# Kernel tuning notes

Measured on AMD Instinct MI355X. Metric: run time of the kernel, lower is better.

## Reference

```python
import jax, jax.numpy as jnp
import numpy as np

B, T, D, H = 2, 2048, 1024, 16
DH = D // H


def setup_inputs() -> dict:
    key = jax.random.key(0)
    ks = jax.random.split(key, 11)
    s = 1.0 / np.sqrt(D)
    return {
        "q": jax.random.normal(ks[0], (B, T, D), jnp.float32),
        "k": jax.random.normal(ks[1], (B, T, D), jnp.float32),
        "v": jax.random.normal(ks[2], (B, T, D), jnp.float32),
        "wq_w": jax.random.normal(ks[3], (D, D), jnp.float32) * s,
        "wq_b": jnp.zeros((D,), jnp.float32),
        "wk_w": jax.random.normal(ks[4], (D, D), jnp.float32) * s,
        "wk_b": jnp.zeros((D,), jnp.float32),
        "wv_w": jax.random.normal(ks[5], (D, D), jnp.float32) * s,
        "wv_b": jnp.zeros((D,), jnp.float32),
        "wo_w": jax.random.normal(ks[6], (D, D), jnp.float32) * s,
        "wo_b": jnp.zeros((D,), jnp.float32),
    }


def reference(q, k, v, wq_w, wq_b, wk_w, wk_b, wv_w, wv_b, wo_w, wo_b):
    b, t, d = q.shape
    # Linear projections (torch Linear: x @ W^T + b)
    wq = (q @ wq_w.T + wq_b).reshape(b, t, H, DH)
    wk = (k @ wk_w.T + wk_b).reshape(b, t, H, DH)
    wv = (v @ wv_w.T + wv_b).reshape(b, t, H, DH)
    # scaled dot-product attention: [b,h,t,s]
    scores = jnp.einsum('bthd,bshd->bhts', wq, wk) / jnp.sqrt(jnp.float32(DH))
    probs = jax.nn.softmax(scores, axis=-1)
    attn = jnp.einsum('bhts,bshd->bthd', probs, wv)  # [b,t,h,dh]
    attn = attn.reshape(b, t, d)
    return attn @ wo_w.T + wo_b
```

## Files before the change

### kernel.cpp

```cpp
#include <hip/hip_runtime.h>
#include <hip/hip_bf16.h>
#include <stdint.h>

#define Bn  2
#define Tn  2048
#define Dn  1024
#define Hn  16
#define DHn 64
#define Mn  (Bn*Tn)

typedef __attribute__((ext_vector_type(8))) short short8;
typedef __attribute__((ext_vector_type(4))) short short4v;
typedef __attribute__((ext_vector_type(4))) float f32x4;

__device__ __forceinline__ f32x4 fzero4() { f32x4 z = {0.f, 0.f, 0.f, 0.f}; return z; }

#define TR16(dst, a32) asm volatile("ds_read_b64_tr_b16 %0, %1" : "=v"(dst) : "v"(a32))

__global__ void cvt4_kernel(const float* __restrict__ a0, const float* __restrict__ a1,
                            const float* __restrict__ a2, const float* __restrict__ a3,
                            __hip_bfloat16* __restrict__ o0, __hip_bfloat16* __restrict__ o1,
                            __hip_bfloat16* __restrict__ o2, __hip_bfloat16* __restrict__ o3, int n)
{
    const int i = (blockIdx.x * blockDim.x + threadIdx.x) * 8;
    if (i >= n) return;
    const float* in = blockIdx.y == 0 ? a0 : (blockIdx.y == 1 ? a1 : (blockIdx.y == 2 ? a2 : a3));
    __hip_bfloat16* out = blockIdx.y == 0 ? o0 : (blockIdx.y == 1 ? o1 : (blockIdx.y == 2 ? o2 : o3));
    float4 a = *(const float4*)(in + i);
    float4 b = *(const float4*)(in + i + 4);
    union { __hip_bfloat16 h[8]; short8 u; } tmp;
    tmp.h[0] = __float2bfloat16(a.x); tmp.h[1] = __float2bfloat16(a.y);
    tmp.h[2] = __float2bfloat16(a.z); tmp.h[3] = __float2bfloat16(a.w);
    tmp.h[4] = __float2bfloat16(b.x); tmp.h[5] = __float2bfloat16(b.y);
    tmp.h[6] = __float2bfloat16(b.z); tmp.h[7] = __float2bfloat16(b.w);
    *(short8*)(out + i) = tmp.u;
}

__global__ __launch_bounds__(256, 3)
void gemm_qkv_kernel(const float* __restrict__ qa, const float* __restrict__ ka,
                     const float* __restrict__ va,
                     const __hip_bfloat16* __restrict__ wq, const __hip_bfloat16* __restrict__ wk,
                     const __hip_bfloat16* __restrict__ wv,
                     const float* __restrict__ bq_, const float* __restrict__ bk_,
                     const float* __restrict__ bv_,
                     __hip_bfloat16* __restrict__ Qp, __hip_bfloat16* __restrict__ Kp,
                     __hip_bfloat16* __restrict__ Vp)
{
    __shared__ alignas(16) short As[2][128*32];
    __shared__ alignas(16) short Bs[2][128*32];
    const int grp = blockIdx.y >> 3;
    const float* A           = grp == 0 ? qa : (grp == 1 ? ka : va);
    const __hip_bfloat16* Bw = grp == 0 ? wq : (grp == 1 ? wk : wv);
    const float* bias        = grp == 0 ? bq_ : (grp == 1 ? bk_ : bv_);
    __hip_bfloat16* C        = grp == 0 ? Qp : (grp == 1 ? Kp : Vp);
    const float scl          = grp == 0 ? 0.18033688011112042f : 1.0f;

    const int t = threadIdx.x, lane = t & 63, wave = t >> 6;
    const int wm = wave >> 1, wn = wave & 1;
    const int row0 = blockIdx.x * 128, col0 = (blockIdx.y & 7) * 128;

    f32x4 acc[4][4];
#pragma unroll
    for (int m = 0; m < 4; ++m)
#pragma unroll
        for (int n = 0; n < 4; ++n) acc[m][n] = fzero4();

    const int srow = wave*16 + (lane >> 2);
    const int skk  = (lane & 3) * 8;
    const int ldsb = wave * 1024 + (lane & 63) * 16;

    float4 ra[2][2];
    auto LOAD_A = [&](int k0) {
#pragma unroll
        for (int i = 0; i < 2; ++i) {
            const float* ap = A + (size_t)(row0 + i*64 + srow)*Dn + k0 + skk;
            ra[i][0] = *(const float4*)ap;
            ra[i][1] = *(const float4*)(ap + 4);
        }
    };
    auto WRITE_A = [&](int buf) {
#pragma unroll
        for (int i = 0; i < 2; ++i) {
            union { __hip_bfloat16 h[8]; short8 u; } w;
            w.h[0] = __float2bfloat16(ra[i][0].x); w.h[1] = __float2bfloat16(ra[i][0].y);
            w.h[2] = __float2bfloat16(ra[i][0].z); w.h[3] = __float2bfloat16(ra[i][0].w);
            w.h[4] = __float2bfloat16(ra[i][1].x); w.h[5] = __float2bfloat16(ra[i][1].y);
            w.h[6] = __float2bfloat16(ra[i][1].z); w.h[7] = __float2bfloat16(ra[i][1].w);
            *(short8*)((char*)As[buf] + i*4096 + ldsb) = w.u;
        }
    };
    auto STAGE_B = [&](int buf, int k0) {
#pragma unroll
        for (int i = 0; i < 2; ++i)
            __builtin_amdgcn_global_load_lds(
                (const __attribute__((address_space(1))) void*)(Bw + (size_t)(col0 + i*64 + srow)*Dn + k0 + skk),
                (__attribute__((address_space(3))) void*)((char*)Bs[buf] + i*4096 + wave*1024 + (lane&63)*16), 16, 0, 0);
    };

    LOAD_A(0);
    STAGE_B(0, 0);
    WRITE_A(0);
    __syncthreads();
    int cur = 0;
    for (int k0 = 0; k0 < Dn; k0 += 32) {
        const bool more = (k0 + 32 < Dn);
        if (more) { LOAD_A(k0 + 32); STAGE_B(cur ^ 1, k0 + 32); }
        short8 af[4], bf_[4];
#pragma unroll
        for (int m = 0; m < 4; ++m)
            af[m] = *(const short8*)((char*)As[cur] + (wm*64 + m*16 + (lane & 15))*64 + (lane >> 4)*16);
#pragma unroll
        for (int n = 0; n < 4; ++n)
            bf_[n] = *(const short8*)((char*)Bs[cur] + (wn*64 + n*16 + (lane & 15))*64 + (lane >> 4)*16);
        __builtin_amdgcn_s_setprio(1);
#pragma unroll
        for (int m = 0; m < 4; ++m)
#pragma unroll
            for (int n = 0; n < 4; ++n)
                acc[m][n] = __builtin_amdgcn_mfma_f32_16x16x32_bf16(af[m], bf_[n], acc[m][n], 0, 0, 0);
        __builtin_amdgcn_s_setprio(0);
        __builtin_amdgcn_sched_barrier(0);
        if (more) WRITE_A(cur ^ 1);
        __syncthreads();
        cur ^= 1;
    }

#pragma unroll
    for (int n = 0; n < 4; ++n) {
        const int col = col0 + wn*64 + n*16 + (lane & 15);
        const float bv = bias[col];
#pragma unroll
        for (int m = 0; m < 4; ++m) {
            const int rb_ = row0 + wm*64 + m*16 + (lane>>4)*4;
#pragma unroll
            for (int i = 0; i < 4; ++i)
                C[(size_t)(rb_+i)*Dn + col] = __float2bfloat16((acc[m][n][i] + bv) * scl);
        }
    }
}

__global__ __launch_bounds__(256, 4)
void gemm_out_kernel(const __hip_bfloat16* __restrict__ A,
                     const __hip_bfloat16* __restrict__ Bw,
                     const float* __restrict__ bias,
                     float* __restrict__ C)
{
    __shared__ alignas(16) short As[2][64*32];
    __shared__ alignas(16) short Bs[2][128*32];
    const int t = threadIdx.x, lane = t & 63, wave = t >> 6;
    const int wm = wave >> 1, wn = wave & 1;
    const int row0 = blockIdx.x * 64, col0 = blockIdx.y * 128;

    f32x4 acc[2][4];
#pragma unroll
    for (int m = 0; m < 2; ++m)
#pragma unroll
        for (int n = 0; n < 4; ++n) acc[m][n] = fzero4();

    const int srow = wave*16 + (lane >> 2);
    const int skk  = (lane & 3) * 8;
    const int ldsb = wave * 1024;

    auto STAGE = [&](int buf, int k0) {
        __builtin_amdgcn_global_load_lds(
            (const __attribute__((address_space(1))) void*)(A + (size_t)(row0 + srow)*Dn + k0 + skk),
            (__attribute__((address_space(3))) void*)((char*)As[buf] + ldsb), 16, 0, 0);
#pragma unroll
        for (int i = 0; i < 2; ++i)
            __builtin_amdgcn_global_load_lds(
                (const __attribute__((address_space(1))) void*)(Bw + (size_t)(col0 + i*64 + srow)*Dn + k0 + skk),
                (__attribute__((address_space(3))) void*)((char*)Bs[buf] + i*4096 + ldsb), 16, 0, 0);
    };

    STAGE(0, 0);
    __syncthreads();
    int cur = 0;
    for (int k0 = 0; k0 < Dn; k0 += 32) {
        if (k0 + 32 < Dn) STAGE(cur ^ 1, k0 + 32);
        short8 af[2], bf_[4];
#pragma unroll
        for (int m = 0; m < 2; ++m)
            af[m] = *(const short8*)((char*)As[cur] + (wm*32 + m*16 + (lane & 15))*64 + (lane >> 4)*16);
#pragma unroll
        for (int n = 0; n < 4; ++n)
            bf_[n] = *(const short8*)((char*)Bs[cur] + (wn*64 + n*16 + (lane & 15))*64 + (lane >> 4)*16);
        __builtin_amdgcn_s_setprio(1);
#pragma unroll
        for (int m = 0; m < 2; ++m)
#pragma unroll
            for (int n = 0; n < 4; ++n)
                acc[m][n] = __builtin_amdgcn_mfma_f32_16x16x32_bf16(af[m], bf_[n], acc[m][n], 0, 0, 0);
        __builtin_amdgcn_s_setprio(0);
        __syncthreads();
        cur ^= 1;
    }

#pragma unroll
    for (int n = 0; n < 4; ++n) {
        const int col = col0 + wn*64 + n*16 + (lane & 15);
        const float bv = bias[col];
#pragma unroll
        for (int m = 0; m < 2; ++m) {
            const int rb_ = row0 + wm*32 + m*16 + (lane>>4)*4;
#pragma unroll
            for (int i = 0; i < 4; ++i)
                C[(size_t)(rb_+i)*Dn + col] = acc[m][n][i] + bv;
        }
    }
}

#define VPL 1288

__global__ __launch_bounds__(256, 2)
void attn_kernel(const __hip_bfloat16* __restrict__ Q,
                 const __hip_bfloat16* __restrict__ K,
                 const __hip_bfloat16* __restrict__ V,
                 __hip_bfloat16* __restrict__ O)
{
    __shared__ alignas(16) short Vlds[2*2*4*VPL];
    const int t = threadIdx.x, lane = t & 63, wave = t >> 6;
    const int g = lane >> 4, c = lane & 15;
    const int pk = wave & 1, qh = wave >> 1;
    const int blk = (blockIdx.x & 7) * 64 + (blockIdx.x >> 3);
    const int qb = blk & 15;
    const int h  = (blk >> 4) & (Hn - 1);
    const int b  = blk >> 8;
    const size_t base = (size_t)b * Tn * Dn + (size_t)h * DHn;
    const int q0 = qb * 128 + qh * 64;

    short8 bq[4][2];
#pragma unroll
    for (int qs = 0; qs < 4; ++qs) {
        const __hip_bfloat16* qp = Q + base + (size_t)(q0 + qs*16 + c) * Dn + g*8;
        bq[qs][0] = *(const short8*)qp;
        bq[qs][1] = *(const short8*)(qp + 32);
    }
    short8 ones;
#pragma unroll
    for (int i = 0; i < 8; ++i) ones[i] = (short)0x3F80;

    f32x4 o_[4][4];
#pragma unroll
    for (int qs = 0; qs < 4; ++qs)
#pragma unroll
        for (int d = 0; d < 4; ++d) o_[qs][d] = fzero4();
    float m_[4] = {-3e38f, -3e38f, -3e38f, -3e38f};
    f32x4 lacc[4] = {fzero4(), fzero4(), fzero4(), fzero4()};

    const int vrow = t >> 3;
    const int vd0  = ((t>>1)&3)*VPL + (vrow>>2)*80 + (vrow&3)*16 + (t&1)*8;
    const int vcol = (((t>>1)&3)*16 + (t&1)*8);
    const uint32_t vbase = (uint32_t)(uintptr_t)(void*)Vlds;
    const uint32_t atr = vbase + (uint32_t)(pk*10304 + g*160 + c*8);

    short8 akA[4][2], akB[4][2];
    {
        const __hip_bfloat16* kp = K + base + (size_t)(pk*64 + c) * Dn + g*8;
#pragma unroll
        for (int sub = 0; sub < 4; ++sub)
#pragma unroll
            for (int ks = 0; ks < 2; ++ks)
                akA[sub][ks] = *(const short8*)(kp + (size_t)sub*16*Dn + ks*32);
    }

    auto ITER = [&](const short8 (&ck)[4][2], short8 (&nk)[4][2], int it) {
        const int kv0 = it * 128;
        short8 cv[2][2];
#pragma unroll
        for (int p = 0; p < 2; ++p) {
            const __hip_bfloat16* vp = V + base + (size_t)(kv0 + p*64 + vrow) * Dn + vcol;
            cv[p][0] = *(const short8*)vp;
            cv[p][1] = *(const short8*)(vp + (size_t)32*Dn);
        }
        {
            const int kvn = (it < 15) ? kv0 + 128 + pk*64 : pk*64;
            const __hip_bfloat16* kp = K + base + (size_t)(kvn + c) * Dn + g*8;
#pragma unroll
            for (int sub = 0; sub < 4; ++sub)
#pragma unroll
                for (int ks = 0; ks < 2; ++ks)
                    nk[sub][ks] = *(const short8*)(kp + (size_t)sub*16*Dn + ks*32);
        }

        short8 pa[4][2];
#pragma unroll
        for (int qs = 0; qs < 4; ++qs) {
            f32x4 s_[4];
#pragma unroll
            for (int sub = 0; sub < 4; ++sub) s_[sub] = fzero4();
            __builtin_amdgcn_s_setprio(1);
#pragma unroll
            for (int sub = 0; sub < 4; ++sub)
#pragma unroll
                for (int ks = 0; ks < 2; ++ks)
                    s_[sub] = __builtin_amdgcn_mfma_f32_16x16x32_bf16(
                        ck[sub][ks], bq[qs][ks], s_[sub], 0, 0, 0);
            __builtin_amdgcn_s_setprio(0);

            float r0 = fmaxf(fmaxf(s_[0][0], s_[0][1]), fmaxf(s_[0][2], s_[0][3]));
            float r1 = fmaxf(fmaxf(s_[1][0], s_[1][1]), fmaxf(s_[1][2], s_[1][3]));
            float r2 = fmaxf(fmaxf(s_[2][0], s_[2][1]), fmaxf(s_[2][2], s_[2][3]));
            float r3 = fmaxf(fmaxf(s_[3][0], s_[3][1]), fmaxf(s_[3][2], s_[3][3]));
            float rm = fmaxf(fmaxf(r0, r1), fmaxf(r2, r3));
            if (!__all(rm - m_[qs] <= 8.0f)) {
                float gm = fmaxf(rm, __shfl_xor(rm, 16));
                gm = fmaxf(gm, __shfl_xor(gm, 32));
                const float mn = fmaxf(m_[qs], gm);
                const float sc = exp2f(m_[qs] - mn);
                m_[qs] = mn;
                lacc[qs][0] *= sc;
#pragma unroll
                for (int d = 0; d < 4; ++d)
#pragma unroll
                    for (int i = 0; i < 4; ++i) o_[qs][d][i] *= sc;
            }
            const float mn = m_[qs];
#pragma unroll
            for (int kc = 0; kc < 2; ++kc)
#pragma unroll
                for (int hf = 0; hf < 2; ++hf)
#pragma unroll
                    for (int i = 0; i < 4; ++i) {
                        const float p = exp2f(s_[kc*2+hf][i] - mn);
                        union { __hip_bfloat16 hb; short u; } cvp;
                        cvp.hb = __float2bfloat16(p);
                        pa[qs][kc][hf*4 + i] = cvp.u;
                    }
            lacc[qs] = __builtin_amdgcn_mfma_f32_16x16x32_bf16(ones, pa[qs][0], lacc[qs], 0, 0, 0);
            lacc[qs] = __builtin_amdgcn_mfma_f32_16x16x32_bf16(ones, pa[qs][1], lacc[qs], 0, 0, 0);
        }

        short* vb = Vlds + (it & 1) * 10304;
#pragma unroll
        for (int p = 0; p < 2; ++p) {
            *(short8*)(vb + p*5152 + vd0)       = cv[p][0];
            *(short8*)(vb + p*5152 + vd0 + 640) = cv[p][1];
        }
        asm volatile("s_waitcnt lgkmcnt(0)" ::: "memory");
        __builtin_amdgcn_s_barrier();
        __builtin_amdgcn_sched_barrier(0);

        const uint32_t atrb = atr + (uint32_t)((it & 1) * 20608u);
        short4v tv[4][2][2];
#pragma unroll
        for (int d = 0; d < 4; ++d)
#pragma unroll
            for (int kc = 0; kc < 2; ++kc) {
                const uint32_t a = atrb + (uint32_t)(d*2576 + kc*1280);
                TR16(tv[d][kc][0], a);
                TR16(tv[d][kc][1], a + 640);
            }
#pragma unroll
        for (int d = 0; d < 4; ++d) {
            if (d == 0)      asm volatile("s_waitcnt lgkmcnt(12)" ::: "memory");
            else if (d == 1) asm volatile("s_waitcnt lgkmcnt(8)" ::: "memory");
            else if (d == 2) asm volatile("s_waitcnt lgkmcnt(4)" ::: "memory");
            else             asm volatile("s_waitcnt lgkmcnt(0)" ::: "memory");
            __builtin_amdgcn_sched_barrier(0);
            const short8 av0 = __builtin_shufflevector(tv[d][0][0], tv[d][0][1], 0,1,2,3,4,5,6,7);
            const short8 av1 = __builtin_shufflevector(tv[d][1][0], tv[d][1][1], 0,1,2,3,4,5,6,7);
            __builtin_amdgcn_s_setprio(1);
#pragma unroll
            for (int qs = 0; qs < 4; ++qs) {
                o_[qs][d] = __builtin_amdgcn_mfma_f32_16x16x32_bf16(av0, pa[qs][0], o_[qs][d], 0, 0, 0);
                o_[qs][d] = __builtin_amdgcn_mfma_f32_16x16x32_bf16(av1, pa[qs][1], o_[qs][d], 0, 0, 0);
            }
            __builtin_amdgcn_s_setprio(0);
        }
    };

    for (int j = 0; j < 8; ++j) {
        ITER(akA, akB, 2*j);
        ITER(akB, akA, 2*j + 1);
    }

    __syncthreads();
    float* cbase = (float*)Vlds;
    if (pk == 1) {
        float* cb = cbase + qh * 4608;
#pragma unroll
        for (int qs = 0; qs < 4; ++qs)
#pragma unroll
            for (int d = 0; d < 4; ++d)
                *(f32x4*)(cb + ((qs*4 + d)*64 + lane)*4) = o_[qs][d];
#pragma unroll
        for (int qs = 0; qs < 4; ++qs) {
            cb[4096 + qs*64 + lane] = m_[qs];
            cb[4352 + qs*64 + lane] = lacc[qs][0];
        }
    }
    __syncthreads();
    if (pk == 0) {
        float* cb = cbase + qh * 4608;
#pragma unroll
        for (int qs = 0; qs < 4; ++qs) {
            const float m1 = cb[4096 + qs*64 + lane];
            const float l1 = cb[4352 + qs*64 + lane];
            const float mN = fmaxf(m_[qs], m1);
            const float sc0 = exp2f(m_[qs] - mN);
            const float sc1 = exp2f(m1 - mN);
            const float inv = 1.f / (lacc[qs][0]*sc0 + l1*sc1);
            __hip_bfloat16* op = O + base + (size_t)(q0 + qs*16 + c) * Dn + g*4;
#pragma unroll
            for (int d = 0; d < 4; ++d) {
                const f32x4 o1 = *(const f32x4*)(cb + ((qs*4 + d)*64 + lane)*4);
                union { __hip_bfloat16 hb[4]; ushort4 u4; } w;
#pragma unroll
                for (int i = 0; i < 4; ++i)
                    w.hb[i] = __float2bfloat16((o_[qs][d][i]*sc0 + o1[i]*sc1) * inv);
                *(ushort4*)(op + d*16) = w.u4;
            }
        }
    }
}

extern "C" void kernel_launch(void* const* d_in, const int* in_sizes, int n_in,
                              void* d_out, int out_size, void* d_ws, size_t ws_size,
                              hipStream_t stream)
{
    (void)in_sizes; (void)n_in; (void)out_size; (void)ws_size;
    const float* q    = (const float*)d_in[0];
    const float* k    = (const float*)d_in[1];
    const float* v    = (const float*)d_in[2];
    const float* wq_w = (const float*)d_in[3];
    const float* wq_b = (const float*)d_in[4];
    const float* wk_w = (const float*)d_in[5];
    const float* wk_b = (const float*)d_in[6];
    const float* wv_w = (const float*)d_in[7];
    const float* wv_b = (const float*)d_in[8];
    const float* wo_w = (const float*)d_in[9];
    const float* wo_b = (const float*)d_in[10];

    char* ws = (char*)d_ws;
    const size_t S1 = (size_t)Mn * Dn * 2;
    const size_t W  = (size_t)Dn * Dn * 2;
    __hip_bfloat16* wqb = (__hip_bfloat16*)(ws);
    __hip_bfloat16* wkb = (__hip_bfloat16*)(ws + W);
    __hip_bfloat16* wvb = (__hip_bfloat16*)(ws + 2*W);
    __hip_bfloat16* wob = (__hip_bfloat16*)(ws + 3*W);
    __hip_bfloat16* Qp  = (__hip_bfloat16*)(ws + 4*W);
    __hip_bfloat16* Kp  = (__hip_bfloat16*)(ws + 4*W + S1);
    __hip_bfloat16* Vp  = (__hip_bfloat16*)(ws + 4*W + 2*S1);
    __hip_bfloat16* Ap  = (__hip_bfloat16*)(ws + 4*W + 3*S1);

    const int nW = Dn * Dn;
    cvt4_kernel<<<dim3(nW/2048, 4), 256, 0, stream>>>(wq_w, wk_w, wv_w, wo_w,
                                                      wqb, wkb, wvb, wob, nW);

    gemm_qkv_kernel<<<dim3(Mn/128, 24), 256, 0, stream>>>(
        q, k, v, wqb, wkb, wvb, wq_b, wk_b, wv_b, Qp, Kp, Vp);

    attn_kernel<<<Bn*Hn*(Tn/128), 256, 0, stream>>>(Qp, Kp, Vp, Ap);

    gemm_out_kernel<<<dim3(Mn/64, Dn/128), 256, 0, stream>>>(Ap, wob, wo_b, (float*)d_out);
}
```

Measured before the change: 134.8 us.

## Split attention KV range across two blocks and merge with combine kernel

Splits each attention block's key/value sequence into two halves, doubling the grid from 512 to 1024 blocks to better fill the GPU's compute units. Each block writes unnormalized fp32 partial outputs plus running max and sum, and a new combine kernel merges the halves and writes bf16 attention output. This trades extra global traffic (fp32 partials, about 33MB written and read back) and an extra kernel launch for more parallelism. The workspace is rearranged so the partials overlap the weight buffers that are no longer needed, and the attention output reuses the Q buffer.

```diff
diff --git a/kernel.cpp b/kernel.cpp
--- a/kernel.cpp
+++ b/kernel.cpp
@@ -215,18 +215,21 @@
 void attn_kernel(const __hip_bfloat16* __restrict__ Q,
                  const __hip_bfloat16* __restrict__ K,
                  const __hip_bfloat16* __restrict__ V,
-                 __hip_bfloat16* __restrict__ O)
+                 float* __restrict__ PO, float* __restrict__ PM, float* __restrict__ PL)
 {
     __shared__ alignas(16) short Vlds[2*2*4*VPL];
     const int t = threadIdx.x, lane = t & 63, wave = t >> 6;
     const int g = lane >> 4, c = lane & 15;
     const int pk = wave & 1, qh = wave >> 1;
-    const int blk = (blockIdx.x & 7) * 64 + (blockIdx.x >> 3);
-    const int qb = blk & 15;
-    const int h  = (blk >> 4) & (Hn - 1);
-    const int b  = blk >> 8;
+    const int blk = (blockIdx.x & 7) * 128 + (blockIdx.x >> 3);
+    const int kvh = blk & 1;
+    const int rest = blk >> 1;
+    const int qb = rest & 15;
+    const int h  = (rest >> 4) & (Hn - 1);
+    const int b  = rest >> 8;
     const size_t base = (size_t)b * Tn * Dn + (size_t)h * DHn;
     const int q0 = qb * 128 + qh * 64;
+    const int kvo = kvh * 1024;
 
     short8 bq[4][2];
 #pragma unroll
@@ -255,7 +258,7 @@
 
     short8 akA[4][2], akB[4][2];
     {
-        const __hip_bfloat16* kp = K + base + (size_t)(pk*64 + c) * Dn + g*8;
+        const __hip_bfloat16* kp = K + base + (size_t)(kvo + pk*64 + c) * Dn + g*8;
 #pragma unroll
         for (int sub = 0; sub < 4; ++sub)
 #pragma unroll
@@ -264,7 +267,7 @@
     }
 
     auto ITER = [&](const short8 (&ck)[4][2], short8 (&nk)[4][2], int it) {
-        const int kv0 = it * 128;
+        const int kv0 = kvo + it * 128;
         short8 cv[2][2];
 #pragma unroll
         for (int p = 0; p < 2; ++p) {
@@ -273,7 +276,7 @@
             cv[p][1] = *(const short8*)(vp + (size_t)32*Dn);
         }
         {
-            const int kvn = (it < 15) ? kv0 + 128 + pk*64 : pk*64;
+            const int kvn = (it < 7) ? kv0 + 128 + pk*64 : kvo + pk*64;
             const __hip_bfloat16* kp = K + base + (size_t)(kvn + c) * Dn + g*8;
 #pragma unroll
             for (int sub = 0; sub < 4; ++sub)
@@ -369,7 +372,7 @@
         }
     };
 
-    for (int j = 0; j < 8; ++j) {
+    for (int j = 0; j < 4; ++j) {
         ITER(akA, akB, 2*j);
         ITER(akB, akA, 2*j + 1);
     }
@@ -392,6 +395,7 @@
     __syncthreads();
     if (pk == 0) {
         float* cb = cbase + qh * 4608;
+        const size_t rowbase = ((size_t)(kvh*Bn + b)*Hn + h)*Tn;
 #pragma unroll
         for (int qs = 0; qs < 4; ++qs) {
             const float m1 = cb[4096 + qs*64 + lane];
@@ -399,19 +403,53 @@
             const float mN = fmaxf(m_[qs], m1);
             const float sc0 = exp2f(m_[qs] - mN);
             const float sc1 = exp2f(m1 - mN);
-            const float inv = 1.f / (lacc[qs][0]*sc0 + l1*sc1);
-            __hip_bfloat16* op = O + base + (size_t)(q0 + qs*16 + c) * Dn + g*4;
+            const float lsum = lacc[qs][0]*sc0 + l1*sc1;
+            const int row = q0 + qs*16 + c;
+            const size_t rowidx = rowbase + row;
+            float* po = PO + rowidx*64;
 #pragma unroll
             for (int d = 0; d < 4; ++d) {
                 const f32x4 o1 = *(const f32x4*)(cb + ((qs*4 + d)*64 + lane)*4);
-                union { __hip_bfloat16 hb[4]; ushort4 u4; } w;
-#pragma unroll
-                for (int i = 0; i < 4; ++i)
-                    w.hb[i] = __float2bfloat16((o_[qs][d][i]*sc0 + o1[i]*sc1) * inv);
-                *(ushort4*)(op + d*16) = w.u4;
+                f32x4 om;
+#pragma unroll
+                for (int i = 0; i < 4; ++i) om[i] = o_[qs][d][i]*sc0 + o1[i]*sc1;
+                *(f32x4*)(po + d*16 + g*4) = om;
             }
-        }
-    }
+            if (g == 0) { PM[rowidx] = mN; PL[rowidx] = lsum; }
+        }
+    }
+}
+
+__global__ void attn_combine_kernel(const float* __restrict__ PO,
+                                    const float* __restrict__ PM,
+                                    const float* __restrict__ PL,
+                                    __hip_bfloat16* __restrict__ Ap)
+{
+    const int tid = blockIdx.x * 256 + threadIdx.x;
+    const int rowq = tid >> 3;
+    const int dh0  = (tid & 7) * 8;
+    const int b = rowq >> 15;
+    const int h = (rowq >> 11) & (Hn - 1);
+    const int q = rowq & (Tn - 1);
+    const size_t r0 = (size_t)rowq;
+    const size_t r1 = r0 + (size_t)Bn * Hn * Tn;
+    const float m0 = PM[r0], m1 = PM[r1];
+    const float l0 = PL[r0], l1 = PL[r1];
+    const float mN = fmaxf(m0, m1);
+    const float sc0 = exp2f(m0 - mN), sc1 = exp2f(m1 - mN);
+    const float inv = 1.f / (l0*sc0 + l1*sc1);
+    const float* p0 = PO + r0*64 + dh0;
+    const float* p1 = PO + r1*64 + dh0;
+    union { __hip_bfloat16 hb[8]; short8 u; } w;
+#pragma unroll
+    for (int j = 0; j < 8; j += 4) {
+        const f32x4 a = *(const f32x4*)(p0 + j);
+        const f32x4 c2 = *(const f32x4*)(p1 + j);
+#pragma unroll
+        for (int i = 0; i < 4; ++i)
+            w.hb[j + i] = __float2bfloat16((a[i]*sc0 + c2[i]*sc1) * inv);
+    }
+    *(short8*)(Ap + ((size_t)b*Tn + q)*Dn + h*64 + dh0) = w.u;
 }
 
 extern "C" void kernel_launch(void* const* d_in, const int* in_sizes, int n_in,
@@ -432,16 +470,22 @@
     const float* wo_b = (const float*)d_in[10];
 
     char* ws = (char*)d_ws;
+    const size_t W  = (size_t)Dn * Dn * 2;
     const size_t S1 = (size_t)Mn * Dn * 2;
-    const size_t W  = (size_t)Dn * Dn * 2;
-    __hip_bfloat16* wqb = (__hip_bfloat16*)(ws);
-    __hip_bfloat16* wkb = (__hip_bfloat16*)(ws + W);
-    __hip_bfloat16* wvb = (__hip_bfloat16*)(ws + 2*W);
-    __hip_bfloat16* wob = (__hip_bfloat16*)(ws + 3*W);
-    __hip_bfloat16* Qp  = (__hip_bfloat16*)(ws + 4*W);
-    __hip_bfloat16* Kp  = (__hip_bfloat16*)(ws + 4*W + S1);
-    __hip_bfloat16* Vp  = (__hip_bfloat16*)(ws + 4*W + 2*S1);
-    __hip_bfloat16* Ap  = (__hip_bfloat16*)(ws + 4*W + 3*S1);
+    const size_t POsz = (size_t)2 * Bn * Hn * Tn * DHn * 4;
+    const size_t MLsz = (size_t)2 * Bn * Hn * Tn * 4;
+
+    __hip_bfloat16* wob = (__hip_bfloat16*)(ws);
+    __hip_bfloat16* Qp  = (__hip_bfloat16*)(ws + W);
+    __hip_bfloat16* Kp  = (__hip_bfloat16*)(ws + W + S1);
+    __hip_bfloat16* Vp  = (__hip_bfloat16*)(ws + W + 2*S1);
+    float* PO = (float*)(ws + W + 3*S1);
+    float* PM = (float*)(ws + W + 3*S1 + POsz);
+    float* PL = (float*)(ws + W + 3*S1 + POsz + MLsz);
+    __hip_bfloat16* wqb = (__hip_bfloat16*)(ws + W + 3*S1);
+    __hip_bfloat16* wkb = (__hip_bfloat16*)(ws + W + 3*S1 + W);
+    __hip_bfloat16* wvb = (__hip_bfloat16*)(ws + W + 3*S1 + 2*W);
+    __hip_bfloat16* Ap  = Qp;
 
     const int nW = Dn * Dn;
     cvt4_kernel<<<dim3(nW/2048, 4), 256, 0, stream>>>(wq_w, wk_w, wv_w, wo_w,
@@ -450,7 +494,9 @@
     gemm_qkv_kernel<<<dim3(Mn/128, 24), 256, 0, stream>>>(
         q, k, v, wqb, wkb, wvb, wq_b, wk_b, wv_b, Qp, Kp, Vp);
 
-    attn_kernel<<<Bn*Hn*(Tn/128), 256, 0, stream>>>(Qp, Kp, Vp, Ap);
+    attn_kernel<<<Bn*Hn*(Tn/128)*2, 256, 0, stream>>>(Qp, Kp, Vp, PO, PM, PL);
+
+    attn_combine_kernel<<<(Bn*Hn*Tn*DHn/8)/256, 256, 0, stream>>>(PO, PM, PL, Ap);
 
     gemm_out_kernel<<<dim3(Mn/64, Dn/128), 256, 0, stream>>>(Ap, wob, wo_b, (float*)d_out);
 }
```

Measured after the change: 146.0 us. 8.3% more time.

## Fuse weight fp32-to-bf16 conversion into GEMM loaders, drop cvt kernel

Applied to the files above, without the earlier changes.

Removes the separate weight conversion kernel and instead has the QKV and output GEMMs load fp32 weights into registers, convert to bf16, and write them into shared memory. This saves one launch and the write-then-reread of bf16 weight copies. In exchange, weights are now read from global memory as fp32 (twice the bytes) repeatedly across many tiles, conversion work is repeated per block, and the async direct-to-LDS path is lost. QKV occupancy hint drops from 3 to 2 to allow the extra registers.

```diff
diff --git a/kernel.cpp b/kernel.cpp
--- a/kernel.cpp
+++ b/kernel.cpp
@@ -17,30 +17,20 @@
 
 #define TR16(dst, a32) asm volatile("ds_read_b64_tr_b16 %0, %1" : "=v"(dst) : "v"(a32))
 
-__global__ void cvt4_kernel(const float* __restrict__ a0, const float* __restrict__ a1,
-                            const float* __restrict__ a2, const float* __restrict__ a3,
-                            __hip_bfloat16* __restrict__ o0, __hip_bfloat16* __restrict__ o1,
-                            __hip_bfloat16* __restrict__ o2, __hip_bfloat16* __restrict__ o3, int n)
-{
-    const int i = (blockIdx.x * blockDim.x + threadIdx.x) * 8;
-    if (i >= n) return;
-    const float* in = blockIdx.y == 0 ? a0 : (blockIdx.y == 1 ? a1 : (blockIdx.y == 2 ? a2 : a3));
-    __hip_bfloat16* out = blockIdx.y == 0 ? o0 : (blockIdx.y == 1 ? o1 : (blockIdx.y == 2 ? o2 : o3));
-    float4 a = *(const float4*)(in + i);
-    float4 b = *(const float4*)(in + i + 4);
-    union { __hip_bfloat16 h[8]; short8 u; } tmp;
-    tmp.h[0] = __float2bfloat16(a.x); tmp.h[1] = __float2bfloat16(a.y);
-    tmp.h[2] = __float2bfloat16(a.z); tmp.h[3] = __float2bfloat16(a.w);
-    tmp.h[4] = __float2bfloat16(b.x); tmp.h[5] = __float2bfloat16(b.y);
-    tmp.h[6] = __float2bfloat16(b.z); tmp.h[7] = __float2bfloat16(b.w);
-    *(short8*)(out + i) = tmp.u;
+__device__ __forceinline__ short8 cvt8(const float4& a, const float4& b) {
+    union { __hip_bfloat16 h[8]; short8 u; } w;
+    w.h[0] = __float2bfloat16(a.x); w.h[1] = __float2bfloat16(a.y);
+    w.h[2] = __float2bfloat16(a.z); w.h[3] = __float2bfloat16(a.w);
+    w.h[4] = __float2bfloat16(b.x); w.h[5] = __float2bfloat16(b.y);
+    w.h[6] = __float2bfloat16(b.z); w.h[7] = __float2bfloat16(b.w);
+    return w.u;
 }
 
-__global__ __launch_bounds__(256, 3)
+__global__ __launch_bounds__(256, 2)
 void gemm_qkv_kernel(const float* __restrict__ qa, const float* __restrict__ ka,
                      const float* __restrict__ va,
-                     const __hip_bfloat16* __restrict__ wq, const __hip_bfloat16* __restrict__ wk,
-                     const __hip_bfloat16* __restrict__ wv,
+                     const float* __restrict__ wq, const float* __restrict__ wk,
+                     const float* __restrict__ wv,
                      const float* __restrict__ bq_, const float* __restrict__ bk_,
                      const float* __restrict__ bv_,
                      __hip_bfloat16* __restrict__ Qp, __hip_bfloat16* __restrict__ Kp,
@@ -49,11 +39,11 @@
     __shared__ alignas(16) short As[2][128*32];
     __shared__ alignas(16) short Bs[2][128*32];
     const int grp = blockIdx.y >> 3;
-    const float* A           = grp == 0 ? qa : (grp == 1 ? ka : va);
-    const __hip_bfloat16* Bw = grp == 0 ? wq : (grp == 1 ? wk : wv);
-    const float* bias        = grp == 0 ? bq_ : (grp == 1 ? bk_ : bv_);
-    __hip_bfloat16* C        = grp == 0 ? Qp : (grp == 1 ? Kp : Vp);
-    const float scl          = grp == 0 ? 0.18033688011112042f : 1.0f;
+    const float* A    = grp == 0 ? qa : (grp == 1 ? ka : va);
+    const float* Bw   = grp == 0 ? wq : (grp == 1 ? wk : wv);
+    const float* bias = grp == 0 ? bq_ : (grp == 1 ? bk_ : bv_);
+    __hip_bfloat16* C = grp == 0 ? Qp : (grp == 1 ? Kp : Vp);
+    const float scl   = grp == 0 ? 0.18033688011112042f : 1.0f;
 
     const int t = threadIdx.x, lane = t & 63, wave = t >> 6;
     const int wm = wave >> 1, wn = wave & 1;
@@ -69,42 +59,31 @@
     const int skk  = (lane & 3) * 8;
     const int ldsb = wave * 1024 + (lane & 63) * 16;
 
-    float4 ra[2][2];
-    auto LOAD_A = [&](int k0) {
+    float4 ra[2][2], rb[2][2];
+    auto LOAD_AB = [&](int k0) {
 #pragma unroll
         for (int i = 0; i < 2; ++i) {
-            const float* ap = A + (size_t)(row0 + i*64 + srow)*Dn + k0 + skk;
-            ra[i][0] = *(const float4*)ap;
-            ra[i][1] = *(const float4*)(ap + 4);
-        }
-    };
-    auto WRITE_A = [&](int buf) {
+            const float* ap = A  + (size_t)(row0 + i*64 + srow)*Dn + k0 + skk;
+            const float* bp = Bw + (size_t)(col0 + i*64 + srow)*Dn + k0 + skk;
+            ra[i][0] = *(const float4*)ap; ra[i][1] = *(const float4*)(ap + 4);
+            rb[i][0] = *(const float4*)bp; rb[i][1] = *(const float4*)(bp + 4);
+        }
+    };
+    auto WRITE_AB = [&](int buf) {
 #pragma unroll
         for (int i = 0; i < 2; ++i) {
-            union { __hip_bfloat16 h[8]; short8 u; } w;
-            w.h[0] = __float2bfloat16(ra[i][0].x); w.h[1] = __float2bfloat16(ra[i][0].y);
-            w.h[2] = __float2bfloat16(ra[i][0].z); w.h[3] = __float2bfloat16(ra[i][0].w);
-            w.h[4] = __float2bfloat16(ra[i][1].x); w.h[5] = __float2bfloat16(ra[i][1].y);
-            w.h[6] = __float2bfloat16(ra[i][1].z); w.h[7] = __float2bfloat16(ra[i][1].w);
-            *(short8*)((char*)As[buf] + i*4096 + ldsb) = w.u;
-        }
-    };
-    auto STAGE_B = [&](int buf, int k0) {
-#pragma unroll
-        for (int i = 0; i < 2; ++i)
-            __builtin_amdgcn_global_load_lds(
-                (const __attribute__((address_space(1))) void*)(Bw + (size_t)(col0 + i*64 + srow)*Dn + k0 + skk),
-                (__attribute__((address_space(3))) void*)((char*)Bs[buf] + i*4096 + wave*1024 + (lane&63)*16), 16, 0, 0);
-    };
-
-    LOAD_A(0);
-    STAGE_B(0, 0);
-    WRITE_A(0);
+            *(short8*)((char*)As[buf] + i*4096 + ldsb) = cvt8(ra[i][0], ra[i][1]);
+            *(short8*)((char*)Bs[buf] + i*4096 + ldsb) = cvt8(rb[i][0], rb[i][1]);
+        }
+    };
+
+    LOAD_AB(0);
+    WRITE_AB(0);
     __syncthreads();
     int cur = 0;
     for (int k0 = 0; k0 < Dn; k0 += 32) {
         const bool more = (k0 + 32 < Dn);
-        if (more) { LOAD_A(k0 + 32); STAGE_B(cur ^ 1, k0 + 32); }
+        if (more) LOAD_AB(k0 + 32);
         short8 af[4], bf_[4];
 #pragma unroll
         for (int m = 0; m < 4; ++m)
@@ -120,7 +99,7 @@
                 acc[m][n] = __builtin_amdgcn_mfma_f32_16x16x32_bf16(af[m], bf_[n], acc[m][n], 0, 0, 0);
         __builtin_amdgcn_s_setprio(0);
         __builtin_amdgcn_sched_barrier(0);
-        if (more) WRITE_A(cur ^ 1);
+        if (more) WRITE_AB(cur ^ 1);
         __syncthreads();
         cur ^= 1;
     }
@@ -141,7 +120,7 @@
 
 __global__ __launch_bounds__(256, 4)
 void gemm_out_kernel(const __hip_bfloat16* __restrict__ A,
-                     const __hip_bfloat16* __restrict__ Bw,
+                     const float* __restrict__ Bw,
                      const float* __restrict__ bias,
                      float* __restrict__ C)
 {
@@ -159,24 +138,35 @@
 
     const int srow = wave*16 + (lane >> 2);
     const int skk  = (lane & 3) * 8;
-    const int ldsb = wave * 1024;
-
-    auto STAGE = [&](int buf, int k0) {
+    const int ldsb = wave * 1024 + (lane & 63) * 16;
+
+    float4 rb[2][2];
+    auto LOAD_B = [&](int k0) {
+#pragma unroll
+        for (int i = 0; i < 2; ++i) {
+            const float* bp = Bw + (size_t)(col0 + i*64 + srow)*Dn + k0 + skk;
+            rb[i][0] = *(const float4*)bp; rb[i][1] = *(const float4*)(bp + 4);
+        }
+    };
+    auto WRITE_B = [&](int buf) {
+#pragma unroll
+        for (int i = 0; i < 2; ++i)
+            *(short8*)((char*)Bs[buf] + i*4096 + ldsb) = cvt8(rb[i][0], rb[i][1]);
+    };
+    auto STAGE_A = [&](int buf, int k0) {
         __builtin_amdgcn_global_load_lds(
             (const __attribute__((address_space(1))) void*)(A + (size_t)(row0 + srow)*Dn + k0 + skk),
-            (__attribute__((address_space(3))) void*)((char*)As[buf] + ldsb), 16, 0, 0);
-#pragma unroll
-        for (int i = 0; i < 2; ++i)
-            __builtin_amdgcn_global_load_lds(
-                (const __attribute__((address_space(1))) void*)(Bw + (size_t)(col0 + i*64 + srow)*Dn + k0 + skk),
-                (__attribute__((address_space(3))) void*)((char*)Bs[buf] + i*4096 + ldsb), 16, 0, 0);
-    };
-
-    STAGE(0, 0);
+            (__attribute__((address_space(3))) void*)((char*)As[buf] + wave*1024 + (lane&63)*16), 16, 0, 0);
+    };
+
+    LOAD_B(0);
+    STAGE_A(0, 0);
+    WRITE_B(0);
     __syncthreads();
     int cur = 0;
     for (int k0 = 0; k0 < Dn; k0 += 32) {
-        if (k0 + 32 < Dn) STAGE(cur ^ 1, k0 + 32);
+        const bool more = (k0 + 32 < Dn);
+        if (more) { LOAD_B(k0 + 32); STAGE_A(cur ^ 1, k0 + 32); }
         short8 af[2], bf_[4];
 #pragma unroll
         for (int m = 0; m < 2; ++m)
@@ -191,6 +181,8 @@
             for (int n = 0; n < 4; ++n)
                 acc[m][n] = __builtin_amdgcn_mfma_f32_16x16x32_bf16(af[m], bf_[n], acc[m][n], 0, 0, 0);
         __builtin_amdgcn_s_setprio(0);
+        __builtin_amdgcn_sched_barrier(0);
+        if (more) WRITE_B(cur ^ 1);
         __syncthreads();
         cur ^= 1;
     }
@@ -433,24 +425,15 @@
 
     char* ws = (char*)d_ws;
     const size_t S1 = (size_t)Mn * Dn * 2;
-    const size_t W  = (size_t)Dn * Dn * 2;
-    __hip_bfloat16* wqb = (__hip_bfloat16*)(ws);
-    __hip_bfloat16* wkb = (__hip_bfloat16*)(ws + W);
-    __hip_bfloat16* wvb = (__hip_bfloat16*)(ws + 2*W);
-    __hip_bfloat16* wob = (__hip_bfloat16*)(ws + 3*W);
-    __hip_bfloat16* Qp  = (__hip_bfloat16*)(ws + 4*W);
-    __hip_bfloat16* Kp  = (__hip_bfloat16*)(ws + 4*W + S1);
-    __hip_bfloat16* Vp  = (__hip_bfloat16*)(ws + 4*W + 2*S1);
-    __hip_bfloat16* Ap  = (__hip_bfloat16*)(ws + 4*W + 3*S1);
-
-    const int nW = Dn * Dn;
-    cvt4_kernel<<<dim3(nW/2048, 4), 256, 0, stream>>>(wq_w, wk_w, wv_w, wo_w,
-                                                      wqb, wkb, wvb, wob, nW);
+    __hip_bfloat16* Qp = (__hip_bfloat16*)(ws);
+    __hip_bfloat16* Kp = (__hip_bfloat16*)(ws + S1);
+    __hip_bfloat16* Vp = (__hip_bfloat16*)(ws + 2*S1);
+    __hip_bfloat16* Ap = (__hip_bfloat16*)(ws + 3*S1);
 
     gemm_qkv_kernel<<<dim3(Mn/128, 24), 256, 0, stream>>>(
-        q, k, v, wqb, wkb, wvb, wq_b, wk_b, wv_b, Qp, Kp, Vp);
+        q, k, v, wq_w, wk_w, wv_w, wq_b, wk_b, wv_b, Qp, Kp, Vp);
 
     attn_kernel<<<Bn*Hn*(Tn/128), 256, 0, stream>>>(Qp, Kp, Vp, Ap);
 
-    gemm_out_kernel<<<dim3(Mn/64, Dn/128), 256, 0, stream>>>(Ap, wob, wo_b, (float*)d_out);
+    gemm_out_kernel<<<dim3(Mn/64, Dn/128), 256, 0, stream>>>(Ap, wo_w, wo_b, (float*)d_out);
 }
```

Measured after the change: 138.0 us. +2.3%, slower.
